# Kernel tuning notes

Measured on AMD Instinct MI355X. Metric: run time of the kernel, lower is better.

Reference implementation:

```python
import jax, jax.numpy as jnp
import numpy as np

K = 20
EPS = 1e-5


def _knn(x, k):
    # x: [B, C, N] -> indices of k nearest points, [B, N, k]
    sq = jnp.sum(x * x, axis=1)  # [B, N]
    neg_d2 = 2.0 * jnp.einsum('bcn,bcm->bnm', x, x) - sq[:, None, :] - sq[:, :, None]
    return jax.lax.top_k(neg_d2, k)[1]


def _graph_feature(x, idx):
    # x: [B, C, N], idx: [B, N, k] -> edge features [B, 2C, N, k]
    xT = x.transpose(0, 2, 1)  # [B, N, C]
    nbr = jax.vmap(lambda t, i: t[i])(xT, idx)  # [B, N, k, C]
    ctr = jnp.broadcast_to(xT[:, :, None, :], nbr.shape)
    f = jnp.concatenate([nbr - ctr, ctr], axis=-1)  # [B, N, k, 2C]
    return f.transpose(0, 3, 1, 2)


def _lrelu(x):
    return jnp.where(x > 0, x, 0.2 * x)


def _bn(x, g, b):
    # eval-mode BatchNorm with freshly-initialized running stats (mean=0, var=1)
    shp = (1, -1) + (1,) * (x.ndim - 2)
    return x * (g / jnp.sqrt(1.0 + EPS)).reshape(shp) + b.reshape(shp)


def _c2(x, w):  # 1x1 Conv2d, no bias
    return jnp.einsum('oi,bink->bonk', w, x)


def _c1(x, w):  # 1x1 Conv1d, no bias
    return jnp.einsum('oi,bin->bon', w, x)


def reference(coords, feats, w1, w2, w3, w4, w5, w6, w7, w8, w9,
              g15, b15, g6, b6, g7, b7, g8, b8):
    x0 = jnp.concatenate([coords.transpose(0, 2, 1), feats], axis=1)  # [B, 6, N]
    n = x0.shape[2]
    # EdgeConv block 1 (kNN on xyz only)
    x = _graph_feature(x0, _knn(x0[:, :3], K))  # [B, 12, N, k]
    x = _lrelu(_bn(_c2(x, w1), g15[0], b15[0]))
    x = _lrelu(_bn(_c2(x, w2), g15[1], b15[1]))
    x1 = jnp.max(x, axis=-1)  # [B, 64, N]
    # EdgeConv block 2 (dynamic kNN in feature space)
    x = _graph_feature(x1, _knn(x1, K))
    x = _lrelu(_bn(_c2(x, w3), g15[2], b15[2]))
    x = _lrelu(_bn(_c2(x, w4), g15[3], b15[3]))
    x2 = jnp.max(x, axis=-1)
    # EdgeConv block 3
    x = _graph_feature(x2, _knn(x2, K))
    x3 = jnp.max(_lrelu(_bn(_c2(x, w5), g15[4], b15[4])), axis=-1)
    # global embedding + per-point head
    xc = jnp.concatenate([x1, x2, x3], axis=1)  # [B, 192, N]
    x = _lrelu(_bn(_c1(xc, w6), g6, b6))  # [B, 1024, N]
    gmax = jnp.max(x, axis=-1, keepdims=True)
    x = jnp.concatenate([jnp.broadcast_to(gmax, (x.shape[0], x.shape[1], n)), x1, x2, x3], axis=1)  # [B,1216,N]
    x = _lrelu(_bn(_c1(x, w7), g7, b7))
    x = _lrelu(_bn(_c1(x, w8), g8, b8))
    # dropout is identity in eval mode
    x = _c1(x, w9)  # [B, 20, N]
    return x.transpose(0, 2, 1).reshape(-1, w9.shape[0])


def setup_inputs() -> dict:
    key = jax.random.key(0)
    ks = jax.random.split(key, 16)
    B, N, C = 8, 4096, 3
    s = 0.1
    return {
        'coords': jax.random.uniform(ks[0], (B, N, 3), jnp.float32),
        'feats': jax.random.normal(ks[1], (B, C, N), jnp.float32),
        'w1': s * jax.random.normal(ks[2], (64, 12), jnp.float32),
        'w2': s * jax.random.normal(ks[3], (64, 64), jnp.float32),
        'w3': s * jax.random.normal(ks[4], (64, 128), jnp.float32),
        'w4': s * jax.random.normal(ks[5], (64, 64), jnp.float32),
        'w5': s * jax.random.normal(ks[6], (64, 128), jnp.float32),
        'w6': s * jax.random.normal(ks[7], (1024, 192), jnp.float32),
        'w7': s * jax.random.normal(ks[8], (512, 1216), jnp.float32),
        'w8': s * jax.random.normal(ks[9], (256, 512), jnp.float32),
        'w9': s * jax.random.normal(ks[10], (20, 256), jnp.float32),
        'g15': jnp.ones((5, 64), jnp.float32),
        'b15': jnp.zeros((5, 64), jnp.float32),
        'g6': jnp.ones((1024,), jnp.float32),
        'b6': jnp.zeros((1024,), jnp.float32),
        'g7': jnp.ones((512,), jnp.float32),
        'b7': jnp.zeros((512,), jnp.float32),
        'g8': jnp.ones((256,), jnp.float32),
        'b8': jnp.zeros((256,), jnp.float32),
    }
```

## Files before the change

kernel.cpp:

```cpp
#include <hip/hip_runtime.h>
#include <math.h>

#define BB 8
#define NN 4096
#define KNN 20
#define EPSBN 1e-5f

__device__ __forceinline__ float lrelu(float x){ return x > 0.f ? x : 0.2f*x; }
__device__ __forceinline__ unsigned encf(float f){
  unsigned u = __float_as_uint(f);
  return (u & 0x80000000u) ? ~u : (u | 0x80000000u);
}
__device__ __forceinline__ float decf(unsigned u){
  return (u & 0x80000000u) ? __uint_as_float(u & 0x7fffffffu) : __uint_as_float(~u);
}
__device__ __forceinline__ float rdlane(float v, int l){
  return __uint_as_float(__builtin_amdgcn_readlane(__float_as_uint(v), l));
}

__global__ void prep_w(float* __restrict__ dst, const float* __restrict__ src,
                       int O, int I, int ld, int coff, const float* __restrict__ g){
  int tot = O*I;
  for(int t = blockIdx.x*blockDim.x + threadIdx.x; t < tot; t += gridDim.x*blockDim.x){
    int o = t % O, i = t / O;
    float s = g ? g[o] * (1.0f/sqrtf(1.0f+EPSBN)) : 1.0f;
    dst[(size_t)i*O + o] = src[(size_t)o*ld + coff + i] * s;
  }
}

__global__ void init_gmax(unsigned* __restrict__ g){
  int t = blockIdx.x*blockDim.x + threadIdx.x;
  if(t < BB*1024) g[t] = 0u;
}

__global__ void build_x0(const float* __restrict__ coords, const float* __restrict__ feats,
                         float* __restrict__ x0p){
  int p = blockIdx.x*blockDim.x + threadIdx.x;
  if(p >= BB*NN) return;
  int b = p / NN, n = p % NN;
  x0p[(size_t)p*6+0] = coords[(size_t)p*3+0];
  x0p[(size_t)p*6+1] = coords[(size_t)p*3+1];
  x0p[(size_t)p*6+2] = coords[(size_t)p*3+2];
  #pragma unroll
  for(int cc=0; cc<3; ++cc) x0p[(size_t)p*6+3+cc] = feats[((size_t)b*3+cc)*NN + n];
}

template<int D, int LD>
__global__ __launch_bounds__(256,3) void knn_kernel(const float* __restrict__ X, int coloff,
                                                    int* __restrict__ idxOut){
  constexpr int IG = 4;
  __shared__ float stage[2][IG][256];
  __shared__ float xi_s[IG][(D+3)&~3];
  __shared__ float sqi_s[IG];
  const int t = threadIdx.x;
  const int b = blockIdx.x / (NN/IG);
  const int i0 = (blockIdx.x % (NN/IG)) * IG;
  const float* Xb = X + (size_t)b*NN*LD + coloff;

  for(int u = t; u < IG*D; u += 256) xi_s[u/D][u%D] = Xb[(size_t)(i0 + u/D)*LD + (u%D)];
  __syncthreads();
  if(t < IG){
    float s = 0.f;
    for(int d=0; d<D; ++d){ float v = xi_s[t][d]; s += v*v; }
    sqi_s[t] = s;
  }
  __syncthreads();

  const int w = t >> 6, l = t & 63;
  float dv[64];
  float cv0=-INFINITY,cv1=-INFINITY,cv2=-INFINITY,cv3=-INFINITY;
  int   cj0=0x7fffffff,cj1=0x7fffffff,cj2=0x7fffffff,cj3=0x7fffffff;

  for(int s = 0; s < NN/256; ++s){
    const int j = s*256 + t;
    const float* row = Xb + (size_t)j*LD;
    float dot0=0.f,dot1=0.f,dot2=0.f,dot3=0.f,sqj=0.f;
    if constexpr (D % 4 == 0){
      #pragma unroll
      for(int d0=0; d0<D; d0+=4){
        const float4 v = *reinterpret_cast<const float4*>(row + d0);
        sqj += v.x*v.x + v.y*v.y + v.z*v.z + v.w*v.w;
        const float4 w0 = *reinterpret_cast<const float4*>(&xi_s[0][d0]);
        const float4 w1 = *reinterpret_cast<const float4*>(&xi_s[1][d0]);
        const float4 w2 = *reinterpret_cast<const float4*>(&xi_s[2][d0]);
        const float4 w3 = *reinterpret_cast<const float4*>(&xi_s[3][d0]);
        dot0 += v.x*w0.x + v.y*w0.y + v.z*w0.z + v.w*w0.w;
        dot1 += v.x*w1.x + v.y*w1.y + v.z*w1.z + v.w*w1.w;
        dot2 += v.x*w2.x + v.y*w2.y + v.z*w2.z + v.w*w2.w;
        dot3 += v.x*w3.x + v.y*w3.y + v.z*w3.z + v.w*w3.w;
      }
    } else {
      #pragma unroll
      for(int d0=0; d0<D; ++d0){
        float v = row[d0];
        sqj += v*v;
        dot0 += v*xi_s[0][d0]; dot1 += v*xi_s[1][d0];
        dot2 += v*xi_s[2][d0]; dot3 += v*xi_s[3][d0];
      }
    }
    const int buf = s & 1;
    stage[buf][0][t] = 2.f*dot0 - sqj - sqi_s[0];
    stage[buf][1][t] = 2.f*dot1 - sqj - sqi_s[1];
    stage[buf][2][t] = 2.f*dot2 - sqj - sqi_s[2];
    stage[buf][3][t] = 2.f*dot3 - sqj - sqi_s[3];
    __syncthreads();
    const float4 v = *reinterpret_cast<const float4*>(&stage[buf][w][4*l]);
    dv[4*s+0]=v.x; dv[4*s+1]=v.y; dv[4*s+2]=v.z; dv[4*s+3]=v.w;
    const int jj = s*256 + 4*l;
    { bool bt = v.x > cv0; cv0 = bt ? v.x : cv0; cj0 = bt ? jj+0 : cj0; }
    { bool bt = v.y > cv1; cv1 = bt ? v.y : cv1; cj1 = bt ? jj+1 : cj1; }
    { bool bt = v.z > cv2; cv2 = bt ? v.z : cv2; cj2 = bt ? jj+2 : cj2; }
    { bool bt = v.w > cv3; cv3 = bt ? v.w : cv3; cj3 = bt ? jj+3 : cj3; }
  }

  int* outRow = idxOut + (size_t)(b*NN + i0 + w)*KNN;
  #pragma unroll 1
  for(int r=0;r<KNN;++r){
    bool c1 = (cv1 > cv0) || (cv1 == cv0 && cj1 < cj0);
    float bv = c1 ? cv1 : cv0; int bj = c1 ? cj1 : cj0;
    bool c2 = (cv3 > cv2) || (cv3 == cv2 && cj3 < cj2);
    float bvB = c2 ? cv3 : cv2; int bjB = c2 ? cj3 : cj2;
    bool c3 = (bvB > bv) || (bvB == bv && bjB < bj);
    bv = c3 ? bvB : bv; bj = c3 ? bjB : bj;
    #pragma unroll
    for(int off = 1; off < 64; off <<= 1){
      float ov = __shfl_xor(bv, off, 64);
      int oj = __shfl_xor(bj, off, 64);
      bool better = (ov > bv) || (ov == bv && oj < bj);
      bv = better ? ov : bv;
      bj = better ? oj : bj;
    }
    if(l == 0) outRow[r] = bj;
    if(l == ((bj >> 2) & 63)){
      const int q = bj & 3;
      dv[4*(bj >> 8) + q] = -INFINITY;
      float nv = -INFINITY; int nj = 0x7fffffff;
      #pragma unroll 1
      for(int s2=0; s2<16; ++s2){
        float vv = dv[4*s2 + q];
        bool bt = vv > nv; nv = bt ? vv : nv; nj = bt ? (s2*256 + 4*l + q) : nj;
      }
      cv0 = (q==0) ? nv : cv0; cj0 = (q==0) ? nj : cj0;
      cv1 = (q==1) ? nv : cv1; cj1 = (q==1) ? nj : cj1;
      cv2 = (q==2) ? nv : cv2; cj2 = (q==2) ? nj : cj2;
      cv3 = (q==3) ? nv : cv3; cj3 = (q==3) ? nj : cj3;
    }
  }
}

template<int DIN, int NL>
__global__ __launch_bounds__(64,3) void edgeconv_k(
    const float* __restrict__ xin, int ldin, int cin_off,
    const int* __restrict__ idx,
    const float* __restrict__ WaT, const float* __restrict__ ba,
    const float* __restrict__ WbT, const float* __restrict__ bb,
    float* __restrict__ xout, int ldout, int cout_off){
  constexpr int PPB = 4;
  const int c = threadIdx.x;
  float wa[DIN];
  #pragma unroll
  for(int d=0; d<DIN; ++d) wa[d] = WaT[d*64 + c];
  float wb[(NL==2)?64:1];
  if constexpr (NL==2){
    #pragma unroll
    for(int d=0; d<64; ++d) wb[d] = WbT[d*64 + c];
  }
  const float bac = ba[c];
  const float bbc = (NL==2) ? bb[c] : 0.f;

  for(int pp=0; pp<PPB; ++pp){
    const int p = blockIdx.x*PPB + pp;
    const int b = p / NN;
    float ctr = (c < DIN) ? xin[(size_t)p*ldin + cin_off + c] : 0.f;
    float bacc[4] = {};
    #pragma unroll
    for(int d=0; d<DIN; ++d)
      bacc[d&3] += rdlane(ctr, d) * (WaT[(DIN+d)*64 + c] - wa[d]);
    const float base = bacc[0]+bacc[1]+bacc[2]+bacc[3];

    const int* irow = idx + (size_t)p*KNN;
    int myidx = (c < KNN) ? irow[c] : 0;
    float vmax = -INFINITY;
    int j0 = __builtin_amdgcn_readlane(myidx, 0);
    float nbr = (c < DIN) ? xin[(size_t)(b*NN + j0)*ldin + cin_off + c] : 0.f;
    for(int k=0; k<KNN; ++k){
      float nbrn = 0.f;
      if(k+1 < KNN){
        int jn = __builtin_amdgcn_readlane(myidx, k+1);
        nbrn = (c < DIN) ? xin[(size_t)(b*NN + jn)*ldin + cin_off + c] : 0.f;
      }
      float hacc[4] = {};
      #pragma unroll
      for(int d=0; d<DIN; ++d) hacc[d&3] += rdlane(nbr, d) * wa[d];
      float a1 = lrelu(base + hacc[0]+hacc[1]+hacc[2]+hacc[3] + bac);
      if constexpr (NL==2){
        float g[4] = {};
        #pragma unroll
        for(int d=0; d<64; ++d) g[d&3] += rdlane(a1, d) * wb[d];
        vmax = fmaxf(vmax, lrelu(g[0]+g[1]+g[2]+g[3] + bbc));
      } else {
        vmax = fmaxf(vmax, a1);
      }
      nbr = nbrn;
    }
    xout[(size_t)p*ldout + cout_off + c] = vmax;
  }
}

template<int EPI>
__global__ __launch_bounds__(256) void gemm_k(
    const float* __restrict__ A, int lda,
    const float* __restrict__ Bm, int Nw, int Ksz,
    const float* __restrict__ bias_n, const float* __restrict__ bias_bn,
    float* __restrict__ C, int ldc, unsigned* __restrict__ gmaxE){
  constexpr int ST = 68;
  __shared__ float At[32*ST];
  __shared__ float Bt[32*ST];
  const int t = threadIdx.x;
  const int m0 = blockIdx.x * 64;
  const int n0 = blockIdx.y * 64;
  const int tm = t >> 4, tn = t & 15;
  float acc[4][4] = {};
  for(int k0 = 0; k0 < Ksz; k0 += 32){
    #pragma unroll
    for(int r=0;r<2;++r){
      int lin = r*256 + t;
      int m = lin >> 3, f4 = lin & 7;
      float4 v = *reinterpret_cast<const float4*>(A + (size_t)(m0+m)*lda + k0 + f4*4);
      At[(f4*4+0)*ST + m] = v.x; At[(f4*4+1)*ST + m] = v.y;
      At[(f4*4+2)*ST + m] = v.z; At[(f4*4+3)*ST + m] = v.w;
    }
    #pragma unroll
    for(int r=0;r<2;++r){
      int lin = r*256 + t;
      int kk = lin >> 4, n4 = lin & 15;
      float4 v = *reinterpret_cast<const float4*>(Bm + (size_t)(k0+kk)*Nw + n0 + n4*4);
      *reinterpret_cast<float4*>(&Bt[kk*ST + n4*4]) = v;
    }
    __syncthreads();
    #pragma unroll
    for(int kk=0; kk<32; ++kk){
      float4 a4 = *reinterpret_cast<const float4*>(&At[kk*ST + tm*4]);
      float4 b4 = *reinterpret_cast<const float4*>(&Bt[kk*ST + tn*4]);
      float av[4] = {a4.x,a4.y,a4.z,a4.w};
      float bw[4] = {b4.x,b4.y,b4.z,b4.w};
      #pragma unroll
      for(int i2=0;i2<4;++i2)
        #pragma unroll
        for(int q=0;q<4;++q) acc[i2][q] += av[i2]*bw[q];
    }
    __syncthreads();
  }
  const int b = m0 / NN;
  if constexpr (EPI == 0){
    float* colm = At;
    #pragma unroll
    for(int q=0;q<4;++q){
      int n = n0 + tn*4 + q;
      float bn = bias_n[n];
      float mx = -INFINITY;
      #pragma unroll
      for(int r2=0;r2<4;++r2) mx = fmaxf(mx, lrelu(acc[r2][q] + bn));
      colm[tm*64 + tn*4 + q] = mx;
    }
    __syncthreads();
    if(t < 64){
      float mx = -INFINITY;
      #pragma unroll
      for(int r2=0;r2<16;++r2) mx = fmaxf(mx, colm[r2*64 + t]);
      atomicMax(gmaxE + b*1024 + n0 + t, encf(mx));
    }
  } else {
    #pragma unroll
    for(int r2=0;r2<4;++r2){
      int row = m0 + tm*4 + r2;
      float4 vo;
      float vv[4];
      #pragma unroll
      for(int q=0;q<4;++q){
        int n = n0 + tn*4 + q;
        float v = acc[r2][q];
        if constexpr (EPI == 1) v += bias_bn[b*512 + n] + bias_n[n];
        else v += bias_n[n];
        vv[q] = lrelu(v);
      }
      vo.x=vv[0]; vo.y=vv[1]; vo.z=vv[2]; vo.w=vv[3];
      *reinterpret_cast<float4*>(C + (size_t)row*ldc + n0 + tn*4) = vo;
    }
  }
}

__global__ __launch_bounds__(256) void bias7_kernel(const unsigned* __restrict__ gmaxE,
    const float* __restrict__ w7, const float* __restrict__ g7, float* __restrict__ b7p){
  __shared__ float gm[1024];
  const int t = threadIdx.x;
  const int b = blockIdx.x, half = blockIdx.y;
  for(int u=t; u<1024; u+=256) gm[u] = decf(gmaxE[b*1024+u]);
  __syncthreads();
  const int o = half*256 + t;
  const float* row = w7 + (size_t)o*1216;
  float acc = 0.f;
  for(int d0=0; d0<1024; d0+=4){
    float4 v = *reinterpret_cast<const float4*>(row + d0);
    acc += v.x*gm[d0] + v.y*gm[d0+1] + v.z*gm[d0+2] + v.w*gm[d0+3];
  }
  b7p[b*512+o] = acc * (g7[o] * (1.0f/sqrtf(1.0f+EPSBN)));
}

__global__ __launch_bounds__(64) void conv9_kernel(const float* __restrict__ y8,
    const float* __restrict__ w9, float* __restrict__ out){
  const int p = blockIdx.x*64 + threadIdx.x;
  float acc[20] = {};
  const float* row = y8 + (size_t)p*256;
  for(int d0=0; d0<256; d0+=4){
    float4 v = *reinterpret_cast<const float4*>(row + d0);
    #pragma unroll
    for(int o=0;o<20;++o){
      float4 w = *reinterpret_cast<const float4*>(w9 + o*256 + d0);
      acc[o] += v.x*w.x + v.y*w.y + v.z*w.z + v.w*w.w;
    }
  }
  #pragma unroll
  for(int o=0;o<20;++o) out[(size_t)p*20+o] = acc[o];
}

extern "C" void kernel_launch(void* const* d_in, const int* in_sizes, int n_in,
                              void* d_out, int out_size, void* d_ws, size_t ws_size,
                              hipStream_t stream){
  const float* coords = (const float*)d_in[0];
  const float* feats  = (const float*)d_in[1];
  const float* w1 = (const float*)d_in[2];
  const float* w2 = (const float*)d_in[3];
  const float* w3 = (const float*)d_in[4];
  const float* w4 = (const float*)d_in[5];
  const float* w5 = (const float*)d_in[6];
  const float* w6 = (const float*)d_in[7];
  const float* w7 = (const float*)d_in[8];
  const float* w8 = (const float*)d_in[9];
  const float* w9 = (const float*)d_in[10];
  const float* g15 = (const float*)d_in[11];
  const float* b15 = (const float*)d_in[12];
  const float* g6 = (const float*)d_in[13];
  const float* b6 = (const float*)d_in[14];
  const float* g7 = (const float*)d_in[15];
  const float* b7 = (const float*)d_in[16];
  const float* g8 = (const float*)d_in[17];
  const float* b8 = (const float*)d_in[18];
  float* out = (float*)d_out;
  float* ws = (float*)d_ws;

  size_t off = 0;
  float* xc   = ws + off; off += (size_t)BB*NN*192;
  float* x0p  = ws + off; off += (size_t)BB*NN*6;
  int*   idx  = (int*)(ws + off); off += (size_t)BB*NN*KNN;
  unsigned* gmaxE = (unsigned*)(ws + off); off += BB*1024;
  float* b7p  = ws + off; off += BB*512;
  float* w1t  = ws + off; off += 12*64;
  float* w2t  = ws + off; off += 64*64;
  float* w3t  = ws + off; off += 128*64;
  float* w4t  = ws + off; off += 64*64;
  float* w5t  = ws + off; off += 128*64;
  float* w6t  = ws + off; off += (size_t)192*1024;
  float* w7lt = ws + off; off += (size_t)192*512;
  float* w8t  = ws + off; off += (size_t)512*256;
  float* y7   = ws + off; off += (size_t)BB*NN*512;
  float* y8   = ws + off; off += (size_t)BB*NN*256;

  auto gb = [](int n){ return dim3((unsigned)((n + 255)/256)); };

  prep_w<<<gb(64*12),  256,0,stream>>>(w1t, w1, 64, 12, 12, 0, g15 + 0);
  prep_w<<<gb(64*64),  256,0,stream>>>(w2t, w2, 64, 64, 64, 0, g15 + 64);
  prep_w<<<gb(64*128), 256,0,stream>>>(w3t, w3, 64, 128, 128, 0, g15 + 128);
  prep_w<<<gb(64*64),  256,0,stream>>>(w4t, w4, 64, 64, 64, 0, g15 + 192);
  prep_w<<<gb(64*128), 256,0,stream>>>(w5t, w5, 64, 128, 128, 0, g15 + 256);
  prep_w<<<gb(1024*192),256,0,stream>>>(w6t, w6, 1024, 192, 192, 0, g6);
  prep_w<<<gb(512*192),256,0,stream>>>(w7lt, w7, 512, 192, 1216, 1024, g7);
  prep_w<<<gb(256*512),256,0,stream>>>(w8t, w8, 256, 512, 512, 0, g8);
  init_gmax<<<gb(BB*1024),256,0,stream>>>(gmaxE);
  build_x0<<<gb(BB*NN),256,0,stream>>>(coords, feats, x0p);

  knn_kernel<3,3><<<BB*(NN/4),256,0,stream>>>(coords, 0, idx);
  edgeconv_k<6,2><<<BB*NN/4,64,0,stream>>>(x0p, 6, 0, idx, w1t, b15+0, w2t, b15+64, xc, 192, 0);
  knn_kernel<64,192><<<BB*(NN/4),256,0,stream>>>(xc, 0, idx);
  edgeconv_k<64,2><<<BB*NN/4,64,0,stream>>>(xc, 192, 0, idx, w3t, b15+128, w4t, b15+192, xc, 192, 64);
  knn_kernel<64,192><<<BB*(NN/4),256,0,stream>>>(xc, 64, idx);
  edgeconv_k<64,1><<<BB*NN/4,64,0,stream>>>(xc, 192, 64, idx, w5t, b15+256, nullptr, nullptr, xc, 192, 128);

  gemm_k<0><<<dim3(BB*NN/64, 1024/64),256,0,stream>>>(xc, 192, w6t, 1024, 192, b6, nullptr, nullptr, 0, gmaxE);
  bias7_kernel<<<dim3(BB,2),256,0,stream>>>(gmaxE, w7, g7, b7p);
  gemm_k<1><<<dim3(BB*NN/64, 512/64),256,0,stream>>>(xc, 192, w7lt, 512, 192, b7, b7p, y7, 512, nullptr);
  gemm_k<2><<<dim3(BB*NN/64, 256/64),256,0,stream>>>(y7, 512, w8t, 256, 512, b8, nullptr, y8, 256, nullptr);
  conv9_kernel<<<BB*NN/64,64,0,stream>>>(y8, w9, out);
}
```

Measured before the change: 4.251 ms.

## Replace per-lane kNN distance cache with top-3 list and rare recompute

The kNN kernel no longer keeps a 64-entry per-thread array of distances. Each lane now keeps a running top-3 of its candidates. When a lane has given up all three, it recomputes its 64 candidate distances from global memory, skipping ones already extracted. The goal is to cut VGPR pressure so more waves fit on each unit and selection costs less. Distance accumulation also switches to explicit fmaf chains. The cost is a divergent, serial recompute path for lanes that hold many true neighbors, plus small numeric differences that can change tie ordering against the reference.

```diff
diff --git a/kernel.cpp b/kernel.cpp
--- a/kernel.cpp
+++ b/kernel.cpp
@@ -53,6 +53,7 @@
   __shared__ float xi_s[IG][(D+3)&~3];
   __shared__ float sqi_s[IG];
   const int t = threadIdx.x;
+  const int w = t >> 6, l = t & 63;
   const int b = blockIdx.x / (NN/IG);
   const int i0 = (blockIdx.x % (NN/IG)) * IG;
   const float* Xb = X + (size_t)b*NN*LD + coloff;
@@ -61,15 +62,23 @@
   __syncthreads();
   if(t < IG){
     float s = 0.f;
-    for(int d=0; d<D; ++d){ float v = xi_s[t][d]; s += v*v; }
+    for(int d=0; d<D; ++d){ float v = xi_s[t][d]; s = fmaf(v, v, s); }
     sqi_s[t] = s;
   }
   __syncthreads();
 
-  const int w = t >> 6, l = t & 63;
-  float dv[64];
-  float cv0=-INFINITY,cv1=-INFINITY,cv2=-INFINITY,cv3=-INFINITY;
-  int   cj0=0x7fffffff,cj1=0x7fffffff,cj2=0x7fffffff,cj3=0x7fffffff;
+  float v1=-INFINITY, v2=-INFINITY, v3=-INFINITY;
+  int   j1=0x7fffffff, j2=0x7fffffff, j3=0x7fffffff;
+
+  auto ins = [&](float v, int jj){
+    bool b1 = v > v1, b2 = v > v2, b3 = v > v3;
+    v3 = b3 ? (b2 ? v2 : v) : v3;
+    j3 = b3 ? (b2 ? j2 : jj) : j3;
+    v2 = b2 ? (b1 ? v1 : v) : v2;
+    j2 = b2 ? (b1 ? j1 : jj) : j2;
+    v1 = b1 ? v : v1;
+    j1 = b1 ? jj : j1;
+  };
 
   for(int s = 0; s < NN/256; ++s){
     const int j = s*256 + t;
@@ -79,23 +88,28 @@
       #pragma unroll
       for(int d0=0; d0<D; d0+=4){
         const float4 v = *reinterpret_cast<const float4*>(row + d0);
-        sqj += v.x*v.x + v.y*v.y + v.z*v.z + v.w*v.w;
+        sqj = fmaf(v.x,v.x,sqj); sqj = fmaf(v.y,v.y,sqj);
+        sqj = fmaf(v.z,v.z,sqj); sqj = fmaf(v.w,v.w,sqj);
         const float4 w0 = *reinterpret_cast<const float4*>(&xi_s[0][d0]);
         const float4 w1 = *reinterpret_cast<const float4*>(&xi_s[1][d0]);
         const float4 w2 = *reinterpret_cast<const float4*>(&xi_s[2][d0]);
         const float4 w3 = *reinterpret_cast<const float4*>(&xi_s[3][d0]);
-        dot0 += v.x*w0.x + v.y*w0.y + v.z*w0.z + v.w*w0.w;
-        dot1 += v.x*w1.x + v.y*w1.y + v.z*w1.z + v.w*w1.w;
-        dot2 += v.x*w2.x + v.y*w2.y + v.z*w2.z + v.w*w2.w;
-        dot3 += v.x*w3.x + v.y*w3.y + v.z*w3.z + v.w*w3.w;
+        dot0 = fmaf(v.x,w0.x,dot0); dot0 = fmaf(v.y,w0.y,dot0);
+        dot0 = fmaf(v.z,w0.z,dot0); dot0 = fmaf(v.w,w0.w,dot0);
+        dot1 = fmaf(v.x,w1.x,dot1); dot1 = fmaf(v.y,w1.y,dot1);
+        dot1 = fmaf(v.z,w1.z,dot1); dot1 = fmaf(v.w,w1.w,dot1);
+        dot2 = fmaf(v.x,w2.x,dot2); dot2 = fmaf(v.y,w2.y,dot2);
+        dot2 = fmaf(v.z,w2.z,dot2); dot2 = fmaf(v.w,w2.w,dot2);
+        dot3 = fmaf(v.x,w3.x,dot3); dot3 = fmaf(v.y,w3.y,dot3);
+        dot3 = fmaf(v.z,w3.z,dot3); dot3 = fmaf(v.w,w3.w,dot3);
       }
     } else {
       #pragma unroll
       for(int d0=0; d0<D; ++d0){
         float v = row[d0];
-        sqj += v*v;
-        dot0 += v*xi_s[0][d0]; dot1 += v*xi_s[1][d0];
-        dot2 += v*xi_s[2][d0]; dot3 += v*xi_s[3][d0];
+        sqj = fmaf(v,v,sqj);
+        dot0 = fmaf(v, xi_s[0][d0], dot0); dot1 = fmaf(v, xi_s[1][d0], dot1);
+        dot2 = fmaf(v, xi_s[2][d0], dot2); dot3 = fmaf(v, xi_s[3][d0], dot3);
       }
     }
     const int buf = s & 1;
@@ -104,24 +118,16 @@
     stage[buf][2][t] = 2.f*dot2 - sqj - sqi_s[2];
     stage[buf][3][t] = 2.f*dot3 - sqj - sqi_s[3];
     __syncthreads();
-    const float4 v = *reinterpret_cast<const float4*>(&stage[buf][w][4*l]);
-    dv[4*s+0]=v.x; dv[4*s+1]=v.y; dv[4*s+2]=v.z; dv[4*s+3]=v.w;
+    const float4 dvv = *reinterpret_cast<const float4*>(&stage[buf][w][4*l]);
     const int jj = s*256 + 4*l;
-    { bool bt = v.x > cv0; cv0 = bt ? v.x : cv0; cj0 = bt ? jj+0 : cj0; }
-    { bool bt = v.y > cv1; cv1 = bt ? v.y : cv1; cj1 = bt ? jj+1 : cj1; }
-    { bool bt = v.z > cv2; cv2 = bt ? v.z : cv2; cj2 = bt ? jj+2 : cj2; }
-    { bool bt = v.w > cv3; cv3 = bt ? v.w : cv3; cj3 = bt ? jj+3 : cj3; }
+    ins(dvv.x, jj+0); ins(dvv.y, jj+1); ins(dvv.z, jj+2); ins(dvv.w, jj+3);
   }
 
   int* outRow = idxOut + (size_t)(b*NN + i0 + w)*KNN;
+  const float sqi = sqi_s[w];
   #pragma unroll 1
   for(int r=0;r<KNN;++r){
-    bool c1 = (cv1 > cv0) || (cv1 == cv0 && cj1 < cj0);
-    float bv = c1 ? cv1 : cv0; int bj = c1 ? cj1 : cj0;
-    bool c2 = (cv3 > cv2) || (cv3 == cv2 && cj3 < cj2);
-    float bvB = c2 ? cv3 : cv2; int bjB = c2 ? cj3 : cj2;
-    bool c3 = (bvB > bv) || (bvB == bv && bjB < bj);
-    bv = c3 ? bvB : bv; bj = c3 ? bjB : bj;
+    float bv = v1; int bj = j1;
     #pragma unroll
     for(int off = 1; off < 64; off <<= 1){
       float ov = __shfl_xor(bv, off, 64);
@@ -131,19 +137,41 @@
       bj = better ? oj : bj;
     }
     if(l == 0) outRow[r] = bj;
-    if(l == ((bj >> 2) & 63)){
-      const int q = bj & 3;
-      dv[4*(bj >> 8) + q] = -INFINITY;
-      float nv = -INFINITY; int nj = 0x7fffffff;
-      #pragma unroll 1
-      for(int s2=0; s2<16; ++s2){
-        float vv = dv[4*s2 + q];
-        bool bt = vv > nv; nv = bt ? vv : nv; nj = bt ? (s2*256 + 4*l + q) : nj;
-      }
-      cv0 = (q==0) ? nv : cv0; cj0 = (q==0) ? nj : cj0;
-      cv1 = (q==1) ? nv : cv1; cj1 = (q==1) ? nj : cj1;
-      cv2 = (q==2) ? nv : cv2; cj2 = (q==2) ? nj : cj2;
-      cv3 = (q==3) ? nv : cv3; cj3 = (q==3) ? nj : cj3;
+    if(((bj >> 2) & 63) == l){
+      const float ve = v1; const int je = j1;
+      v1=v2; j1=j2; v2=v3; j2=j3; v3=-INFINITY; j3=0x7fffffff;
+      if(j1 == 0x7fffffff){
+        #pragma unroll 1
+        for(int s2=0; s2<16; ++s2){
+          #pragma unroll
+          for(int q=0; q<4; ++q){
+            const int jj = s2*256 + 4*l + q;
+            const float* rowp = Xb + (size_t)jj*LD;
+            float dot=0.f, sqj=0.f;
+            if constexpr (D % 4 == 0){
+              #pragma unroll 4
+              for(int d0=0; d0<D; d0+=4){
+                const float4 v = *reinterpret_cast<const float4*>(rowp + d0);
+                sqj = fmaf(v.x,v.x,sqj); sqj = fmaf(v.y,v.y,sqj);
+                sqj = fmaf(v.z,v.z,sqj); sqj = fmaf(v.w,v.w,sqj);
+                const float4 xw = *reinterpret_cast<const float4*>(&xi_s[w][d0]);
+                dot = fmaf(v.x,xw.x,dot); dot = fmaf(v.y,xw.y,dot);
+                dot = fmaf(v.z,xw.z,dot); dot = fmaf(v.w,xw.w,dot);
+              }
+            } else {
+              #pragma unroll
+              for(int d0=0; d0<D; ++d0){
+                float v = rowp[d0];
+                sqj = fmaf(v,v,sqj);
+                dot = fmaf(v, xi_s[w][d0], dot);
+              }
+            }
+            const float dq = 2.f*dot - sqj - sqi;
+            const bool ok = (dq < ve) || (dq == ve && jj > je);
+            if(ok) ins(dq, jj);
+          }
+        }
+      }
     }
   }
 }
```

Measured after the change: 4.070 ms. 1.04x faster.
